# Performance work log

Measured on AMD Instinct MI355X. Metric: run time of the kernel, lower is better.

## Reference

```python
import jax, jax.numpy as jnp
import numpy as np

B, DIM, H, W = 4, 192, 128, 128
HEADS = 4
K_RATES = (1.0 / 2, 2.0 / 3, 3.0 / 4, 4.0 / 5)


def setup_inputs() -> dict:
    key = jax.random.key(0)
    ks = jax.random.split(key, 5)
    x = jax.random.normal(ks[0], (B, DIM, H, W), jnp.float32)
    w_qkv = jax.random.normal(ks[1], (3 * DIM, DIM, 1, 1), jnp.float32) * 0.05
    w_dw = jax.random.normal(ks[2], (3 * DIM, 1, 3, 3), jnp.float32) * 0.05
    w_proj = jax.random.normal(ks[3], (DIM, DIM, 1, 1), jnp.float32) * 0.05
    temperature = jnp.ones((HEADS, 1, 1), jnp.float32)
    attn_w = jnp.full((4,), 0.2, jnp.float32)
    return {"x": x, "w_qkv": w_qkv, "w_dw": w_dw, "w_proj": w_proj,
            "temperature": temperature, "attn_w": attn_w}


def _conv1x1(x, w):
    # x: [b,c,h,w], w: [o,c,1,1]
    return jnp.einsum('bchw,oc->bohw', x, w[:, :, 0, 0])


def _dwconv3x3(x, w):
    # depthwise 3x3, padding=1; w: [c,1,3,3]
    return jax.lax.conv_general_dilated(
        x, w, window_strides=(1, 1), padding=((1, 1), (1, 1)),
        dimension_numbers=('NCHW', 'OIHW', 'NCHW'),
        feature_group_count=x.shape[1])


def _l2norm(x, eps=1e-12):
    # matches F.normalize(dim=-1): x / max(||x||, eps)
    n = jnp.sqrt(jnp.sum(x * x, axis=-1, keepdims=True))
    return x / jnp.maximum(n, eps)


def reference(x, w_qkv, w_dw, w_proj, temperature, attn_w):
    b, c, h, w = x.shape
    qkv = _dwconv3x3(_conv1x1(x, w_qkv), w_dw)  # [b, 3c, h, w]
    q, k, v = jnp.split(qkv, 3, axis=1)

    def heads(t):
        return t.reshape(b, HEADS, c // HEADS, h * w)  # [b, head, C, hw]

    q, k, v = heads(q), heads(k), heads(v)
    q = _l2norm(q)
    k = _l2norm(k)

    C = q.shape[2]
    attn = jnp.einsum('bhcn,bhdn->bhcd', q, k) * temperature[None]  # [b,head,C,C]

    out = jnp.zeros_like(v)
    for i, rate in enumerate(K_RATES):
        k_val = max(1, int(C * rate))
        _, idx = jax.lax.top_k(attn, k_val)  # [b,head,C,k]
        mask = jax.nn.one_hot(idx, C, dtype=attn.dtype).sum(axis=-2)  # [b,head,C,C]
        branch = jnp.where(mask > 0, attn, -jnp.inf)
        branch = jax.nn.softmax(branch, axis=-1)
        out = out + jnp.einsum('bhcd,bhdn->bhcn', branch, v) * attn_w[i]

    out = out.reshape(b, c, h, w)
    return _conv1x1(out, w_proj)
```

## Files before the change

### kernel.cpp

```cpp
#include <hip/hip_runtime.h>
#include <math.h>
#include <stdint.h>

#define BB 4
#define DIM 192
#define HEADS 4
#define CH 48
#define HW 16384
#define C3 576
#define NCHUNK 64

typedef unsigned short ushort_t;
typedef __attribute__((ext_vector_type(8))) short short8;
typedef __attribute__((ext_vector_type(4))) float floatx4;

__device__ __forceinline__ float bf2f(unsigned int u) {
    union { unsigned int i; float f; } v; v.i = u << 16; return v.f;
}
__device__ __forceinline__ ushort_t f2bf(float f) {
    union { float f; unsigned int i; } v; v.f = f;
    unsigned int x = v.i;
    x += 0x7fffu + ((x >> 16) & 1u);
    return (ushort_t)(x >> 16);
}

__global__ __launch_bounds__(256) void zero_init(float* __restrict__ p, int n) {
    int i = blockIdx.x * 256 + threadIdx.x;
    if (i < n) p[i] = 0.f;
}

__global__ __launch_bounds__(256) void convert_split(
    const float* __restrict__ in, ushort_t* __restrict__ hi,
    ushort_t* __restrict__ lo, int n)
{
    int i = blockIdx.x * 256 + threadIdx.x;
    if (i < n) {
        float f = in[i];
        ushort_t h = f2bf(f);
        hi[i] = h;
        lo[i] = f2bf(f - bf2f(h));
    }
}

__global__ __launch_bounds__(256) void tconv(
    const float* __restrict__ in, ushort_t* __restrict__ out_hi,
    ushort_t* __restrict__ out_lo, int wlo, long inStride)
{
    int z = blockIdx.z;
    in += (long)z * inStride;
    out_hi += (long)z * HW * DIM;
    if (wlo) out_lo += (long)z * HW * DIM;
    __shared__ ushort_t th[64][80];
    __shared__ ushort_t tl[64][80];
    int n0 = blockIdx.x * 64, k0 = blockIdx.y * 64;
    int t = threadIdx.x;
#pragma unroll
    for (int i = 0; i < 4; ++i) {
        int kl = (t >> 4) + 16 * i;
        float4 v = *(const float4*)(in + (long)(k0 + kl) * HW + n0 + (t & 15) * 4);
        int nl = (t & 15) * 4;
        ushort_t hx = f2bf(v.x), hy = f2bf(v.y), hz = f2bf(v.z), hw = f2bf(v.w);
        th[nl + 0][kl] = hx; th[nl + 1][kl] = hy;
        th[nl + 2][kl] = hz; th[nl + 3][kl] = hw;
        if (wlo) {
            tl[nl + 0][kl] = f2bf(v.x - bf2f(hx));
            tl[nl + 1][kl] = f2bf(v.y - bf2f(hy));
            tl[nl + 2][kl] = f2bf(v.z - bf2f(hz));
            tl[nl + 3][kl] = f2bf(v.w - bf2f(hw));
        }
    }
    __syncthreads();
#pragma unroll
    for (int i = 0; i < 2; ++i) {
        int nl = t >> 2, seg = (t & 3) + 4 * i;
        *(uint4*)(out_hi + (long)(n0 + nl) * DIM + k0 + seg * 8) = *(uint4*)&th[nl][seg * 8];
        if (wlo)
            *(uint4*)(out_lo + (long)(n0 + nl) * DIM + k0 + seg * 8) = *(uint4*)&tl[nl][seg * 8];
    }
}

#define BS_STRIDE 104
template<int TERMS>
__global__ __launch_bounds__(256) void gemm_reg(
    const ushort_t* __restrict__ Ahi, const ushort_t* __restrict__ Alo,
    const ushort_t* __restrict__ BThi, const ushort_t* __restrict__ BTlo,
    float* __restrict__ C, int M, int N,
    long strideA, long strideB, long strideC)
{
    int z = blockIdx.z;
    Ahi += z * strideA; Alo += z * strideA;
    BThi += z * strideB; BTlo += z * strideB;
    C += z * strideC;
    __shared__ ushort_t Bs0[128 * BS_STRIDE];
    __shared__ ushort_t Bs1[128 * BS_STRIDE];
    int t = threadIdx.x;
    int wave = t >> 6, lane = t & 63;
    int l15 = lane & 15, quad = lane >> 4;
    int m0 = blockIdx.y * 64, n0 = blockIdx.x * 128;
    int wm = (wave & 1) * 32, wn = (wave >> 1) * 64;
    floatx4 acc[2][4];
#pragma unroll
    for (int i = 0; i < 2; ++i)
#pragma unroll
        for (int j = 0; j < 4; ++j) acc[i][j] = (floatx4){0.f, 0.f, 0.f, 0.f};

    if (TERMS == 1) {
        short8 af[2][6];
#pragma unroll
        for (int mi = 0; mi < 2; ++mi)
#pragma unroll
            for (int k0 = 0; k0 < 6; ++k0)
                af[mi][k0] = *(const short8*)(Ahi
                    + (long)(m0 + wm + mi * 16 + l15) * 192 + k0 * 32 + quad * 8);
        for (int i = t; i < 3072; i += 256) {
            int r = i / 24, seg = i % 24;
            uint4 v = *(const uint4*)(BThi + (long)(n0 + r) * 192 + seg * 8);
            ushort_t* dst = (seg < 12) ? &Bs0[r * BS_STRIDE + seg * 8]
                                       : &Bs1[r * BS_STRIDE + (seg - 12) * 8];
            *(uint4*)dst = v;
        }
        __syncthreads();
#pragma unroll
        for (int k0 = 0; k0 < 6; ++k0) {
            int ks = k0 * 32 + quad * 8;
            const ushort_t* buf = (ks < 96) ? Bs0 : Bs1;
            int col = (ks < 96) ? ks : ks - 96;
            short8 bf[4];
#pragma unroll
            for (int ni = 0; ni < 4; ++ni)
                bf[ni] = *(const short8*)&buf[(wn + ni * 16 + l15) * BS_STRIDE + col];
#pragma unroll
            for (int mi = 0; mi < 2; ++mi)
#pragma unroll
                for (int ni = 0; ni < 4; ++ni)
                    acc[mi][ni] = __builtin_amdgcn_mfma_f32_16x16x32_bf16(
                        af[mi][k0], bf[ni], acc[mi][ni], 0, 0, 0);
        }
    } else {
#pragma unroll
        for (int kh = 0; kh < 2; ++kh) {
            short8 ah[2][3], al[2][3];
#pragma unroll
            for (int mi = 0; mi < 2; ++mi)
#pragma unroll
                for (int k0 = 0; k0 < 3; ++k0) {
                    long off = (long)(m0 + wm + mi * 16 + l15) * 192
                             + kh * 96 + k0 * 32 + quad * 8;
                    ah[mi][k0] = *(const short8*)(Ahi + off);
                    al[mi][k0] = *(const short8*)(Alo + off);
                }
            if (kh) __syncthreads();
            for (int i = t; i < 1536; i += 256) {
                int r = i / 12, seg = i % 12;
                long goff = (long)(n0 + r) * 192 + kh * 96 + seg * 8;
                *(uint4*)&Bs0[r * BS_STRIDE + seg * 8] = *(const uint4*)(BThi + goff);
                *(uint4*)&Bs1[r * BS_STRIDE + seg * 8] = *(const uint4*)(BTlo + goff);
            }
            __syncthreads();
#pragma unroll
            for (int k0 = 0; k0 < 3; ++k0) {
                int col = k0 * 32 + quad * 8;
                short8 bh[4], bl[4];
#pragma unroll
                for (int ni = 0; ni < 4; ++ni) {
                    bh[ni] = *(const short8*)&Bs0[(wn + ni * 16 + l15) * BS_STRIDE + col];
                    bl[ni] = *(const short8*)&Bs1[(wn + ni * 16 + l15) * BS_STRIDE + col];
                }
#pragma unroll
                for (int mi = 0; mi < 2; ++mi)
#pragma unroll
                    for (int ni = 0; ni < 4; ++ni) {
                        acc[mi][ni] = __builtin_amdgcn_mfma_f32_16x16x32_bf16(
                            ah[mi][k0], bh[ni], acc[mi][ni], 0, 0, 0);
                        acc[mi][ni] = __builtin_amdgcn_mfma_f32_16x16x32_bf16(
                            ah[mi][k0], bl[ni], acc[mi][ni], 0, 0, 0);
                        acc[mi][ni] = __builtin_amdgcn_mfma_f32_16x16x32_bf16(
                            al[mi][k0], bh[ni], acc[mi][ni], 0, 0, 0);
                    }
            }
        }
    }
#pragma unroll
    for (int mi = 0; mi < 2; ++mi)
#pragma unroll
        for (int ni = 0; ni < 4; ++ni) {
            long base = (long)(m0 + wm + mi * 16 + quad * 4) * N + n0 + wn + ni * 16 + l15;
#pragma unroll
            for (int r = 0; r < 4; ++r)
                C[base + (long)r * N] = acc[mi][ni][r];
        }
}

__global__ __launch_bounds__(256) void dwconv3x3_lds(
    const float* __restrict__ in, const float* __restrict__ w,
    ushort_t* __restrict__ qk_hi, ushort_t* __restrict__ qk_lo,
    float* __restrict__ vbuf, float* __restrict__ normsq,
    int c0, int chunk)
{
    __shared__ float tile[10][132];
    int z = blockIdx.z;
    int cl = blockIdx.y;
    int gc = c0 + cl;
    in  += (long)z * chunk * HW + (long)cl * HW;
    int y0 = blockIdx.x * 8;
    const float* wc = w + gc * 9;
    float wf[9];
#pragma unroll
    for (int i = 0; i < 9; ++i) wf[i] = wc[i];
    int t = threadIdx.x;
    if (t < 10) { tile[t][0] = 0.f; tile[t][129] = 0.f; }
    for (int i = t; i < 320; i += 256) {
        int r = i >> 5, c4 = (i & 31) * 4;
        int gy = y0 - 1 + r;
        float4 v = {0.f, 0.f, 0.f, 0.f};
        if (gy >= 0 && gy < 128) v = *(const float4*)(in + gy * 128 + c4);
        tile[r][1 + c4] = v.x; tile[r][2 + c4] = v.y;
        tile[r][3 + c4] = v.z; tile[r][4 + c4] = v.w;
    }
    __syncthreads();
    int yl = t >> 5, xl = (t & 31) * 4;
    float s0 = 0.f, s1 = 0.f, s2 = 0.f, s3 = 0.f;
#pragma unroll
    for (int r = 0; r < 3; ++r) {
        float c0v = tile[yl + r][xl + 0], c1v = tile[yl + r][xl + 1];
        float c2v = tile[yl + r][xl + 2], c3v = tile[yl + r][xl + 3];
        float c4v = tile[yl + r][xl + 4], c5v = tile[yl + r][xl + 5];
        float w0 = wf[r * 3], w1 = wf[r * 3 + 1], w2 = wf[r * 3 + 2];
        s0 += w0 * c0v + w1 * c1v + w2 * c2v;
        s1 += w0 * c1v + w1 * c2v + w2 * c3v;
        s2 += w0 * c2v + w1 * c3v + w2 * c4v;
        s3 += w0 * c3v + w1 * c4v + w2 * c5v;
    }
    long pix = (long)(y0 + yl) * 128 + xl;
    if (gc < 2 * DIM) {
        ushort_t h0 = f2bf(s0), h1 = f2bf(s1), h2 = f2bf(s2), h3 = f2bf(s3);
        ushort_t l0 = f2bf(s0 - bf2f(h0)), l1 = f2bf(s1 - bf2f(h1));
        ushort_t l2 = f2bf(s2 - bf2f(h2)), l3 = f2bf(s3 - bf2f(h3));
        uint2 ph, pl;
        ph.x = (unsigned)h0 | ((unsigned)h1 << 16);
        ph.y = (unsigned)h2 | ((unsigned)h3 << 16);
        pl.x = (unsigned)l0 | ((unsigned)l1 << 16);
        pl.y = (unsigned)l2 | ((unsigned)l3 << 16);
        long rbase = ((long)z * 384 + gc) * HW + pix;
        *(uint2*)(qk_hi + rbase) = ph;
        *(uint2*)(qk_lo + rbase) = pl;
        __syncthreads();
        float* red = (float*)tile;
        red[t] = s0 * s0 + s1 * s1 + s2 * s2 + s3 * s3;
        __syncthreads();
        for (int off = 128; off > 0; off >>= 1) {
            if (t < off) red[t] += red[t + off];
            __syncthreads();
        }
        if (t == 0) atomicAdd(&normsq[z * 512 + gc], red[0]);
    } else {
        float4 o = {s0, s1, s2, s3};
        *(float4*)(vbuf + ((long)z * DIM + (gc - 2 * DIM)) * HW + pix) = o;
    }
}

__global__ __launch_bounds__(256) void attn_mfma(
    const ushort_t* __restrict__ qk_hi, const ushort_t* __restrict__ qk_lo,
    float* __restrict__ partial)
{
    int z = blockIdx.z, h = blockIdx.y, pidx = blockIdx.x;
    int t = threadIdx.x;
    int wave = t >> 6, lane = t & 63;
    int l15 = lane & 15, quad = lane >> 4;
    long base = (long)z * 384 * HW;
    const ushort_t* qh = qk_hi + base + (long)(h * CH) * HW;
    const ushort_t* ql = qk_lo + base + (long)(h * CH) * HW;
    const ushort_t* kh = qk_hi + base + (long)(DIM + h * CH) * HW;
    const ushort_t* kl = qk_lo + base + (long)(DIM + h * CH) * HW;
    int ncol0 = pidx * 256 + wave * 64;

    floatx4 acc[3][3];
#pragma unroll
    for (int i = 0; i < 3; ++i)
#pragma unroll
        for (int j = 0; j < 3; ++j) acc[i][j] = (floatx4){0.f, 0.f, 0.f, 0.f};

#pragma unroll
    for (int ks = 0; ks < 2; ++ks) {
        int col = ncol0 + ks * 32 + quad * 8;
        short8 ah[3], al[3], bh[3], bl[3];
#pragma unroll
        for (int i = 0; i < 3; ++i) {
            long ro = (long)(i * 16 + l15) * HW + col;
            ah[i] = *(const short8*)(qh + ro);
            al[i] = *(const short8*)(ql + ro);
            bh[i] = *(const short8*)(kh + ro);
            bl[i] = *(const short8*)(kl + ro);
        }
#pragma unroll
        for (int mi = 0; mi < 3; ++mi)
#pragma unroll
            for (int ni = 0; ni < 3; ++ni) {
                acc[mi][ni] = __builtin_amdgcn_mfma_f32_16x16x32_bf16(
                    ah[mi], bh[ni], acc[mi][ni], 0, 0, 0);
                acc[mi][ni] = __builtin_amdgcn_mfma_f32_16x16x32_bf16(
                    ah[mi], bl[ni], acc[mi][ni], 0, 0, 0);
                acc[mi][ni] = __builtin_amdgcn_mfma_f32_16x16x32_bf16(
                    al[mi], bh[ni], acc[mi][ni], 0, 0, 0);
            }
    }

    __shared__ float sred[2][48 * 50];
    float* sb = sred[wave & 1];
    if (wave < 2) {
#pragma unroll
        for (int mi = 0; mi < 3; ++mi)
#pragma unroll
            for (int ni = 0; ni < 3; ++ni)
#pragma unroll
                for (int r = 0; r < 4; ++r)
                    sb[(mi * 16 + quad * 4 + r) * 50 + ni * 16 + l15] = acc[mi][ni][r];
    }
    __syncthreads();
    if (wave >= 2) {
#pragma unroll
        for (int mi = 0; mi < 3; ++mi)
#pragma unroll
            for (int ni = 0; ni < 3; ++ni)
#pragma unroll
                for (int r = 0; r < 4; ++r)
                    sb[(mi * 16 + quad * 4 + r) * 50 + ni * 16 + l15] += acc[mi][ni][r];
    }
    __syncthreads();
    float* pp = partial + ((long)(pidx * 16 + z * HEADS + h)) * 2304;
    for (int i = t; i < 2304; i += 256) {
        int row = i / 48, colo = i - row * 48;
        pp[i] = sred[0][row * 50 + colo] + sred[1][row * 50 + colo];
    }
}

__global__ __launch_bounds__(256) void topk_combine2(
    const float* __restrict__ partial, const float* __restrict__ normsq,
    const float* __restrict__ temp, const float* __restrict__ attn_w,
    float* __restrict__ Wc)
{
    int z = blockIdx.y;
    int wave = threadIdx.x >> 6, lane = threadIdx.x & 63;
    int rid = blockIdx.x * 4 + wave;
    int c = rid % CH, h = rid / CH;
    int d = lane;
    float a = -INFINITY;
    if (d < 48) {
        float s = 0.f;
        const float* pp = partial + (long)(z * HEADS + h) * 2304 + c * CH + d;
        for (int p = 0; p < NCHUNK; ++p) s += pp[(long)p * 16 * 2304];
        float invq = 1.0f / fmaxf(sqrtf(normsq[z * 512 + h * CH + c]), 1e-12f);
        float invk = 1.0f / fmaxf(sqrtf(normsq[z * 512 + DIM + h * CH + d]), 1e-12f);
        a = s * invq * invk * temp[h];
    }
    float m = a;
#pragma unroll
    for (int off = 32; off > 0; off >>= 1) m = fmaxf(m, __shfl_xor(m, off, 64));
    float e = (d < 48) ? expf(a - m) : 0.f;
    int rank = 0;
    for (int j = 0; j < 48; ++j) {
        float aj = __shfl(a, j, 64);
        rank += (aj > a) || (aj == a && j < d);
    }
    const int kv[4] = {24, 32, 36, 38};
    float s = 0.f;
#pragma unroll
    for (int i = 0; i < 4; ++i) {
        float contrib = (d < 48 && rank < kv[i]) ? e : 0.f;
#pragma unroll
        for (int off = 32; off > 0; off >>= 1) contrib += __shfl_xor(contrib, off, 64);
        s += (rank < kv[i]) ? attn_w[i] / contrib : 0.f;
    }
    if (d < 48) Wc[(long)z * 9216 + (long)rid * CH + d] = e * s;
}

__global__ __launch_bounds__(256) void build_m(
    const float* __restrict__ wproj, const float* __restrict__ Wc,
    ushort_t* __restrict__ Mb)
{
    int z = blockIdx.y;
    int idx = blockIdx.x * 256 + threadIdx.x;
    if (idx >= DIM * DIM) return;
    int cg = idx % DIM;
    int o  = idx / DIM;
    int h = cg / CH, d = cg % CH;
    const float* wp = wproj + o * DIM + h * CH;
    const float* wcc = Wc + (long)z * 9216 + (long)h * CH * CH + d;
    float s = 0.f;
#pragma unroll
    for (int ch = 0; ch < CH; ++ch) s += wp[ch] * wcc[ch * CH];
    Mb[(long)z * DIM * DIM + idx] = f2bf(s);
}

extern "C" void kernel_launch(void* const* d_in, const int* in_sizes, int n_in,
                              void* d_out, int out_size, void* d_ws, size_t ws_size,
                              hipStream_t stream) {
    const float* x      = (const float*)d_in[0];
    const float* w_qkv  = (const float*)d_in[1];
    const float* w_dw   = (const float*)d_in[2];
    const float* w_proj = (const float*)d_in[3];
    const float* temper = (const float*)d_in[4];
    const float* attn_w = (const float*)d_in[5];
    float* out = (float*)d_out;

    char* p = (char*)d_ws;
    ushort_t* qk_hi  = (ushort_t*)p;   p += (long)BB * 384 * HW * 2;
    ushort_t* qk_lo  = (ushort_t*)p;   p += (long)BB * 384 * HW * 2;
    float* vbuf      = (float*)p;      p += (long)BB * DIM * HW * 4;
    ushort_t* xT_hi  = (ushort_t*)p;   p += (long)BB * HW * DIM * 2;
    ushort_t* xT_lo  = (ushort_t*)p;   p += (long)BB * HW * DIM * 2;
    ushort_t* wq_hi  = (ushort_t*)p;   p += (long)C3 * DIM * 2;
    ushort_t* wq_lo  = (ushort_t*)p;   p += (long)C3 * DIM * 2;
    float* normsq    = (float*)p;      p += (long)BB * 512 * 4;
    float* Wc        = (float*)p;      p += (long)BB * 9216 * 4;
    ushort_t* Mb     = (ushort_t*)p;   p += (long)BB * DIM * DIM * 2;
    float* pre       = (float*)p;
    float* partial   = pre;
    long avail = (long)ws_size - (long)(p - (char*)d_ws);
    int chunk = 64;
    if (avail >= (long)BB * 192 * HW * 4) chunk = 192;

    zero_init<<<(BB * 512 + 255) / 256, 256, 0, stream>>>(normsq, BB * 512);
    convert_split<<<(C3 * DIM + 255) / 256, 256, 0, stream>>>(
        w_qkv, wq_hi, wq_lo, C3 * DIM);
    tconv<<<dim3(HW / 64, DIM / 64, BB), 256, 0, stream>>>(
        x, xT_hi, xT_lo, 1, (long)DIM * HW);

    for (int c0 = 0; c0 < C3; c0 += chunk) {
        if (c0 < 2 * DIM)
            gemm_reg<3><<<dim3(HW / 128, chunk / 64, BB), 256, 0, stream>>>(
                wq_hi + (long)c0 * DIM, wq_lo + (long)c0 * DIM, xT_hi, xT_lo,
                pre, chunk, HW, 0L, (long)HW * DIM, (long)chunk * HW);
        else
            gemm_reg<1><<<dim3(HW / 128, chunk / 64, BB), 256, 0, stream>>>(
                wq_hi + (long)c0 * DIM, wq_hi + (long)c0 * DIM, xT_hi, xT_hi,
                pre, chunk, HW, 0L, (long)HW * DIM, (long)chunk * HW);
        dwconv3x3_lds<<<dim3(16, chunk, BB), 256, 0, stream>>>(
            pre, w_dw, qk_hi, qk_lo, vbuf, normsq, c0, chunk);
    }
    attn_mfma<<<dim3(NCHUNK, HEADS, BB), 256, 0, stream>>>(qk_hi, qk_lo, partial);
    topk_combine2<<<dim3(48, BB), 256, 0, stream>>>(
        partial, normsq, temper, attn_w, Wc);
    build_m<<<dim3((DIM * DIM + 255) / 256, BB), 256, 0, stream>>>(w_proj, Wc, Mb);
    tconv<<<dim3(HW / 64, DIM / 64, BB), 256, 0, stream>>>(
        vbuf, xT_hi, xT_lo, 0, (long)DIM * HW);
    gemm_reg<1><<<dim3(HW / 128, DIM / 64, BB), 256, 0, stream>>>(
        Mb, Mb, xT_hi, xT_hi, out, DIM, HW,
        (long)DIM * DIM, (long)HW * DIM, (long)DIM * HW);
}
```

Measured before the change: 381.8 us.

## Store V as bf16 and shrink GEMM N-tile to 64 columns

The depthwise conv now writes the V channels directly as bf16 instead of fp32, and a new bf16-to-bf16 transpose kernel replaces the fp32 transpose for V. This halves V write and read traffic and drops the lo-term branch from tconv. Separately, the GEMM N tile is halved from 128 to 64, which doubles the block count, cuts LDS per block and lowers register pressure, at the cost of more A-operand reloads per output. Rounding V to bf16 happens earlier but matches what the final GEMM already used.

```diff
diff --git a/kernel.cpp b/kernel.cpp
--- a/kernel.cpp
+++ b/kernel.cpp
@@ -44,12 +44,12 @@
 
 __global__ __launch_bounds__(256) void tconv(
     const float* __restrict__ in, ushort_t* __restrict__ out_hi,
-    ushort_t* __restrict__ out_lo, int wlo, long inStride)
+    ushort_t* __restrict__ out_lo, long inStride)
 {
     int z = blockIdx.z;
     in += (long)z * inStride;
     out_hi += (long)z * HW * DIM;
-    if (wlo) out_lo += (long)z * HW * DIM;
+    out_lo += (long)z * HW * DIM;
     __shared__ ushort_t th[64][80];
     __shared__ ushort_t tl[64][80];
     int n0 = blockIdx.x * 64, k0 = blockIdx.y * 64;
@@ -62,20 +62,44 @@
         ushort_t hx = f2bf(v.x), hy = f2bf(v.y), hz = f2bf(v.z), hw = f2bf(v.w);
         th[nl + 0][kl] = hx; th[nl + 1][kl] = hy;
         th[nl + 2][kl] = hz; th[nl + 3][kl] = hw;
-        if (wlo) {
-            tl[nl + 0][kl] = f2bf(v.x - bf2f(hx));
-            tl[nl + 1][kl] = f2bf(v.y - bf2f(hy));
-            tl[nl + 2][kl] = f2bf(v.z - bf2f(hz));
-            tl[nl + 3][kl] = f2bf(v.w - bf2f(hw));
-        }
+        tl[nl + 0][kl] = f2bf(v.x - bf2f(hx));
+        tl[nl + 1][kl] = f2bf(v.y - bf2f(hy));
+        tl[nl + 2][kl] = f2bf(v.z - bf2f(hz));
+        tl[nl + 3][kl] = f2bf(v.w - bf2f(hw));
     }
     __syncthreads();
 #pragma unroll
     for (int i = 0; i < 2; ++i) {
         int nl = t >> 2, seg = (t & 3) + 4 * i;
         *(uint4*)(out_hi + (long)(n0 + nl) * DIM + k0 + seg * 8) = *(uint4*)&th[nl][seg * 8];
-        if (wlo)
-            *(uint4*)(out_lo + (long)(n0 + nl) * DIM + k0 + seg * 8) = *(uint4*)&tl[nl][seg * 8];
+        *(uint4*)(out_lo + (long)(n0 + nl) * DIM + k0 + seg * 8) = *(uint4*)&tl[nl][seg * 8];
+    }
+}
+
+__global__ __launch_bounds__(256) void tconv_b16(
+    const ushort_t* __restrict__ in, ushort_t* __restrict__ out)
+{
+    int z = blockIdx.z;
+    in  += (long)z * DIM * HW;
+    out += (long)z * HW * DIM;
+    __shared__ ushort_t th[64][80];
+    int n0 = blockIdx.x * 64, k0 = blockIdx.y * 64;
+    int t = threadIdx.x;
+#pragma unroll
+    for (int i = 0; i < 4; ++i) {
+        int kl = (t >> 4) + 16 * i;
+        uint2 v = *(const uint2*)(in + (long)(k0 + kl) * HW + n0 + (t & 15) * 4);
+        int nl = (t & 15) * 4;
+        th[nl + 0][kl] = (ushort_t)(v.x & 0xffffu);
+        th[nl + 1][kl] = (ushort_t)(v.x >> 16);
+        th[nl + 2][kl] = (ushort_t)(v.y & 0xffffu);
+        th[nl + 3][kl] = (ushort_t)(v.y >> 16);
+    }
+    __syncthreads();
+#pragma unroll
+    for (int i = 0; i < 2; ++i) {
+        int nl = t >> 2, seg = (t & 3) + 4 * i;
+        *(uint4*)(out + (long)(n0 + nl) * DIM + k0 + seg * 8) = *(uint4*)&th[nl][seg * 8];
     }
 }
 
@@ -91,18 +115,18 @@
     Ahi += z * strideA; Alo += z * strideA;
     BThi += z * strideB; BTlo += z * strideB;
     C += z * strideC;
-    __shared__ ushort_t Bs0[128 * BS_STRIDE];
-    __shared__ ushort_t Bs1[128 * BS_STRIDE];
+    __shared__ ushort_t Bs0[64 * BS_STRIDE];
+    __shared__ ushort_t Bs1[64 * BS_STRIDE];
     int t = threadIdx.x;
     int wave = t >> 6, lane = t & 63;
     int l15 = lane & 15, quad = lane >> 4;
-    int m0 = blockIdx.y * 64, n0 = blockIdx.x * 128;
-    int wm = (wave & 1) * 32, wn = (wave >> 1) * 64;
-    floatx4 acc[2][4];
+    int m0 = blockIdx.y * 64, n0 = blockIdx.x * 64;
+    int wm = (wave & 1) * 32, wn = (wave >> 1) * 32;
+    floatx4 acc[2][2];
 #pragma unroll
     for (int i = 0; i < 2; ++i)
 #pragma unroll
-        for (int j = 0; j < 4; ++j) acc[i][j] = (floatx4){0.f, 0.f, 0.f, 0.f};
+        for (int j = 0; j < 2; ++j) acc[i][j] = (floatx4){0.f, 0.f, 0.f, 0.f};
 
     if (TERMS == 1) {
         short8 af[2][6];
@@ -112,7 +136,7 @@
             for (int k0 = 0; k0 < 6; ++k0)
                 af[mi][k0] = *(const short8*)(Ahi
                     + (long)(m0 + wm + mi * 16 + l15) * 192 + k0 * 32 + quad * 8);
-        for (int i = t; i < 3072; i += 256) {
+        for (int i = t; i < 1536; i += 256) {
             int r = i / 24, seg = i % 24;
             uint4 v = *(const uint4*)(BThi + (long)(n0 + r) * 192 + seg * 8);
             ushort_t* dst = (seg < 12) ? &Bs0[r * BS_STRIDE + seg * 8]
@@ -125,14 +149,14 @@
             int ks = k0 * 32 + quad * 8;
             const ushort_t* buf = (ks < 96) ? Bs0 : Bs1;
             int col = (ks < 96) ? ks : ks - 96;
-            short8 bf[4];
-#pragma unroll
-            for (int ni = 0; ni < 4; ++ni)
+            short8 bf[2];
+#pragma unroll
+            for (int ni = 0; ni < 2; ++ni)
                 bf[ni] = *(const short8*)&buf[(wn + ni * 16 + l15) * BS_STRIDE + col];
 #pragma unroll
             for (int mi = 0; mi < 2; ++mi)
 #pragma unroll
-                for (int ni = 0; ni < 4; ++ni)
+                for (int ni = 0; ni < 2; ++ni)
                     acc[mi][ni] = __builtin_amdgcn_mfma_f32_16x16x32_bf16(
                         af[mi][k0], bf[ni], acc[mi][ni], 0, 0, 0);
         }
@@ -150,7 +174,7 @@
                     al[mi][k0] = *(const short8*)(Alo + off);
                 }
             if (kh) __syncthreads();
-            for (int i = t; i < 1536; i += 256) {
+            for (int i = t; i < 768; i += 256) {
                 int r = i / 12, seg = i % 12;
                 long goff = (long)(n0 + r) * 192 + kh * 96 + seg * 8;
                 *(uint4*)&Bs0[r * BS_STRIDE + seg * 8] = *(const uint4*)(BThi + goff);
@@ -160,16 +184,16 @@
 #pragma unroll
             for (int k0 = 0; k0 < 3; ++k0) {
                 int col = k0 * 32 + quad * 8;
-                short8 bh[4], bl[4];
-#pragma unroll
-                for (int ni = 0; ni < 4; ++ni) {
+                short8 bh[2], bl[2];
+#pragma unroll
+                for (int ni = 0; ni < 2; ++ni) {
                     bh[ni] = *(const short8*)&Bs0[(wn + ni * 16 + l15) * BS_STRIDE + col];
                     bl[ni] = *(const short8*)&Bs1[(wn + ni * 16 + l15) * BS_STRIDE + col];
                 }
 #pragma unroll
                 for (int mi = 0; mi < 2; ++mi)
 #pragma unroll
-                    for (int ni = 0; ni < 4; ++ni) {
+                    for (int ni = 0; ni < 2; ++ni) {
                         acc[mi][ni] = __builtin_amdgcn_mfma_f32_16x16x32_bf16(
                             ah[mi][k0], bh[ni], acc[mi][ni], 0, 0, 0);
                         acc[mi][ni] = __builtin_amdgcn_mfma_f32_16x16x32_bf16(
@@ -183,7 +207,7 @@
 #pragma unroll
     for (int mi = 0; mi < 2; ++mi)
 #pragma unroll
-        for (int ni = 0; ni < 4; ++ni) {
+        for (int ni = 0; ni < 2; ++ni) {
             long base = (long)(m0 + wm + mi * 16 + quad * 4) * N + n0 + wn + ni * 16 + l15;
 #pragma unroll
             for (int r = 0; r < 4; ++r)
@@ -194,7 +218,7 @@
 __global__ __launch_bounds__(256) void dwconv3x3_lds(
     const float* __restrict__ in, const float* __restrict__ w,
     ushort_t* __restrict__ qk_hi, ushort_t* __restrict__ qk_lo,
-    float* __restrict__ vbuf, float* __restrict__ normsq,
+    ushort_t* __restrict__ vbuf16, float* __restrict__ normsq,
     int c0, int chunk)
 {
     __shared__ float tile[10][132];
@@ -232,13 +256,14 @@
         s3 += w0 * c3v + w1 * c4v + w2 * c5v;
     }
     long pix = (long)(y0 + yl) * 128 + xl;
+    ushort_t h0 = f2bf(s0), h1 = f2bf(s1), h2 = f2bf(s2), h3 = f2bf(s3);
+    uint2 ph;
+    ph.x = (unsigned)h0 | ((unsigned)h1 << 16);
+    ph.y = (unsigned)h2 | ((unsigned)h3 << 16);
     if (gc < 2 * DIM) {
-        ushort_t h0 = f2bf(s0), h1 = f2bf(s1), h2 = f2bf(s2), h3 = f2bf(s3);
         ushort_t l0 = f2bf(s0 - bf2f(h0)), l1 = f2bf(s1 - bf2f(h1));
         ushort_t l2 = f2bf(s2 - bf2f(h2)), l3 = f2bf(s3 - bf2f(h3));
-        uint2 ph, pl;
-        ph.x = (unsigned)h0 | ((unsigned)h1 << 16);
-        ph.y = (unsigned)h2 | ((unsigned)h3 << 16);
+        uint2 pl;
         pl.x = (unsigned)l0 | ((unsigned)l1 << 16);
         pl.y = (unsigned)l2 | ((unsigned)l3 << 16);
         long rbase = ((long)z * 384 + gc) * HW + pix;
@@ -254,8 +279,7 @@
         }
         if (t == 0) atomicAdd(&normsq[z * 512 + gc], red[0]);
     } else {
-        float4 o = {s0, s1, s2, s3};
-        *(float4*)(vbuf + ((long)z * DIM + (gc - 2 * DIM)) * HW + pix) = o;
+        *(uint2*)(vbuf16 + ((long)z * DIM + (gc - 2 * DIM)) * HW + pix) = ph;
     }
 }
 
@@ -406,7 +430,7 @@
     char* p = (char*)d_ws;
     ushort_t* qk_hi  = (ushort_t*)p;   p += (long)BB * 384 * HW * 2;
     ushort_t* qk_lo  = (ushort_t*)p;   p += (long)BB * 384 * HW * 2;
-    float* vbuf      = (float*)p;      p += (long)BB * DIM * HW * 4;
+    ushort_t* vbuf16 = (ushort_t*)p;   p += (long)BB * DIM * HW * 2;
     ushort_t* xT_hi  = (ushort_t*)p;   p += (long)BB * HW * DIM * 2;
     ushort_t* xT_lo  = (ushort_t*)p;   p += (long)BB * HW * DIM * 2;
     ushort_t* wq_hi  = (ushort_t*)p;   p += (long)C3 * DIM * 2;
@@ -424,27 +448,26 @@
     convert_split<<<(C3 * DIM + 255) / 256, 256, 0, stream>>>(
         w_qkv, wq_hi, wq_lo, C3 * DIM);
     tconv<<<dim3(HW / 64, DIM / 64, BB), 256, 0, stream>>>(
-        x, xT_hi, xT_lo, 1, (long)DIM * HW);
+        x, xT_hi, xT_lo, (long)DIM * HW);
 
     for (int c0 = 0; c0 < C3; c0 += chunk) {
         if (c0 < 2 * DIM)
-            gemm_reg<3><<<dim3(HW / 128, chunk / 64, BB), 256, 0, stream>>>(
+            gemm_reg<3><<<dim3(HW / 64, chunk / 64, BB), 256, 0, stream>>>(
                 wq_hi + (long)c0 * DIM, wq_lo + (long)c0 * DIM, xT_hi, xT_lo,
                 pre, chunk, HW, 0L, (long)HW * DIM, (long)chunk * HW);
         else
-            gemm_reg<1><<<dim3(HW / 128, chunk / 64, BB), 256, 0, stream>>>(
+            gemm_reg<1><<<dim3(HW / 64, chunk / 64, BB), 256, 0, stream>>>(
                 wq_hi + (long)c0 * DIM, wq_hi + (long)c0 * DIM, xT_hi, xT_hi,
                 pre, chunk, HW, 0L, (long)HW * DIM, (long)chunk * HW);
         dwconv3x3_lds<<<dim3(16, chunk, BB), 256, 0, stream>>>(
-            pre, w_dw, qk_hi, qk_lo, vbuf, normsq, c0, chunk);
+            pre, w_dw, qk_hi, qk_lo, vbuf16, normsq, c0, chunk);
     }
     attn_mfma<<<dim3(NCHUNK, HEADS, BB), 256, 0, stream>>>(qk_hi, qk_lo, partial);
     topk_combine2<<<dim3(48, BB), 256, 0, stream>>>(
         partial, normsq, temper, attn_w, Wc);
     build_m<<<dim3((DIM * DIM + 255) / 256, BB), 256, 0, stream>>>(w_proj, Wc, Mb);
-    tconv<<<dim3(HW / 64, DIM / 64, BB), 256, 0, stream>>>(
-        vbuf, xT_hi, xT_lo, 0, (long)DIM * HW);
-    gemm_reg<1><<<dim3(HW / 128, DIM / 64, BB), 256, 0, stream>>>(
+    tconv_b16<<<dim3(HW / 64, DIM / 64, BB), 256, 0, stream>>>(vbuf16, xT_hi);
+    gemm_reg<1><<<dim3(HW / 64, DIM / 64, BB), 256, 0, stream>>>(
         Mb, Mb, xT_hi, xT_hi, out, DIM, HW,
         (long)DIM * DIM, (long)HW * DIM, (long)DIM * HW);
 }
```

Measured after the change: 392.6 us. 2.8% more time.
